# Kernel optimization log

Hardware: AMD Instinct MI355X
Metric: run time of the kernel (lower is better)

## Reference

```python
import jax, jax.numpy as jnp
import numpy as np

SCALE_REACH = 10.0   # 'scale' in forward
SCALE_COS = 16.0     # CosNorm_Classifier default scale


def setup_inputs() -> dict:
    key = jax.random.key(0)
    ks = jax.random.split(key, 7)
    B, C, F = 64, 1000, 2048
    return {
        "x": jax.random.normal(ks[0], (B, F), jnp.float32),
        "centroids": jax.random.normal(ks[1], (C, F), jnp.float32),
        "W_hall": jax.random.normal(ks[2], (C, F), jnp.float32) * 0.02,
        "b_hall": jax.random.normal(ks[3], (C,), jnp.float32) * 0.02,
        "W_sel": jax.random.normal(ks[4], (F, F), jnp.float32) * 0.02,
        "b_sel": jax.random.normal(ks[5], (F,), jnp.float32) * 0.02,
        "W_cos": jax.random.normal(ks[6], (C, F), jnp.float32) * 0.001,
    }


def reference(x, centroids, W_hall, b_hall, W_sel, b_sel, W_cos):
    direct_feature = x
    # L2 distance to every class centroid: [B, C] (materializes [B, C, F] diff as in torch)
    diff = x[:, None, :] - centroids[None, :, :]
    dist = jnp.sqrt(jnp.sum(diff * diff, axis=2))
    # original sorts then takes column 0 -> min distance
    min_dist = jnp.min(dist, axis=1)                      # [B]
    reachability = (SCALE_REACH / min_dist)[:, None]      # [B, 1], broadcast over feat

    # hallucinated memory read
    values_memory = jax.nn.softmax(x @ W_hall.T + b_hall, axis=1)  # [B, C]
    memory_feature = values_memory @ centroids                      # [B, F]

    concept_selector = jnp.tanh(x @ W_sel.T + b_sel)                # [B, F]
    infused_feature = concept_selector * memory_feature
    feat = reachability * (direct_feature + infused_feature)

    # CosNorm classifier
    norm_x = jnp.linalg.norm(feat, axis=1, keepdims=True)           # [B, 1]
    ex = (norm_x / (1.0 + norm_x)) * (feat / norm_x)                # norm-gated unit vec
    ew = W_cos / jnp.linalg.norm(W_cos, axis=1, keepdims=True)      # [C, F]
    logits = ex @ (ew.T * SCALE_COS)                                # [B, C]

    return logits, direct_feature, infused_feature
```

## Files before the change

kernel.cpp:

```cpp
#include <hip/hip_runtime.h>
#include <math.h>

#define FF 2048

typedef __attribute__((ext_vector_type(8))) short short8;
typedef __attribute__((ext_vector_type(4))) float floatx4;

#define OFF_SPART 0
#define OFF_HPART 1024000
#define OFF_SELP  2048000
#define OFF_MEMP  4145152
#define OFF_LOGP  5193728
#define OFF_V     7241728
#define OFF_FEAT  7307264
#define OFF_CN2   7438336
#define OFF_WINV  7439336
#define OFF_XN2   7440336
#define OFF_REACH 7440400
#define OFF_NRM2P 7440464

#define TP 40

__device__ __forceinline__ void split2(float f, ushort& h, ushort& l) {
  unsigned u = __float_as_uint(f);
  float r = f - __uint_as_float(u & 0xffff0000u);
  h = (ushort)(u >> 16);
  l = (ushort)(__float_as_uint(r) >> 16);
}

struct R2 { float4 a, b; };

__device__ __forceinline__ void load_bt(const float* __restrict__ M, int ldK, int rowBase,
                                        int nrows, int k0, R2& s, int t) {
  int r = t >> 2, q = t & 3;
  int grow = rowBase + r;
  const float* src = M + (size_t)grow * ldK + k0 + q * 8;
  s.a = make_float4(0.f, 0.f, 0.f, 0.f);
  s.b = s.a;
  if (grow < nrows) {
    s.a = *(const float4*)src;
    s.b = *(const float4*)(src + 4);
  }
}

__device__ __forceinline__ void store_bt(const R2& s, ushort* __restrict__ hi,
                                         ushort* __restrict__ lo, int t) {
  int r = t >> 2, q = t & 3;
#pragma unroll
  for (int h = 0; h < 2; ++h) {
    const float4& v = h ? s.b : s.a;
    ushort4 hv, lv;
    split2(v.x, hv.x, lv.x); split2(v.y, hv.y, lv.y);
    split2(v.z, hv.z, lv.z); split2(v.w, hv.w, lv.w);
    int base = r * TP + q * 8 + h * 4;
    *(ushort4*)(hi + base) = hv;
    *(ushort4*)(lo + base) = lv;
  }
}

__device__ __forceinline__ void load_tr(const float* __restrict__ M, int ldN, int k0, int kmax,
                                        int n0, R2& s, int t) {
  int kk = t >> 3, c8 = (t & 7) * 8;
  int gk = k0 + kk;
  const float* src = M + (size_t)gk * ldN + n0 + c8;
  s.a = make_float4(0.f, 0.f, 0.f, 0.f);
  s.b = s.a;
  if (gk < kmax) {
    s.a = *(const float4*)src;
    s.b = *(const float4*)(src + 4);
  }
}

__device__ __forceinline__ void store_tr(const R2& s, ushort* __restrict__ hi,
                                         ushort* __restrict__ lo, int t) {
  int kk = t >> 3, c8 = (t & 7) * 8;
#pragma unroll
  for (int j = 0; j < 8; ++j) {
    float f = (j < 4) ? ((const float*)&s.a)[j] : ((const float*)&s.b)[j - 4];
    ushort h, l;
    split2(f, h, l);
    hi[(c8 + j) * TP + kk] = h;
    lo[(c8 + j) * TP + kk] = l;
  }
}

#define MFMA(a, b, c) __builtin_amdgcn_mfma_f32_16x16x32_bf16(a, b, c, 0, 0, 0)

__device__ __forceinline__ void mfma_tile(const ushort* __restrict__ Ah, const ushort* __restrict__ Al,
                                          const ushort* __restrict__ Bh, const ushort* __restrict__ Bl,
                                          int ln15, int q8, int mh, int nh, floatx4 (&acc)[2][2]) {
  short8 ah[2], al[2];
#pragma unroll
  for (int i = 0; i < 2; ++i) {
    int row = (mh * 2 + i) * 16 + ln15;
    ah[i] = *(const short8*)(Ah + row * TP + q8);
    al[i] = *(const short8*)(Al + row * TP + q8);
  }
#pragma unroll
  for (int j = 0; j < 2; ++j) {
    int brow = (nh * 2 + j) * 16 + ln15;
    short8 bh = *(const short8*)(Bh + brow * TP + q8);
    short8 bl = *(const short8*)(Bl + brow * TP + q8);
#pragma unroll
    for (int i = 0; i < 2; ++i) {
      acc[i][j] = MFMA(ah[i], bh, acc[i][j]);
      acc[i][j] = MFMA(ah[i], bl, acc[i][j]);
      acc[i][j] = MFMA(al[i], bh, acc[i][j]);
    }
  }
}

__global__ __launch_bounds__(256) void k1_gemm1(
    const float* __restrict__ x, const float* __restrict__ cent,
    const float* __restrict__ whall, const float* __restrict__ wcos,
    float* __restrict__ ws) {
  __shared__ __align__(16) ushort u_lds[4 * 64 * TP];
  ushort* Ah = u_lds;
  ushort* Al = u_lds + 64 * TP;
  ushort* Bh = u_lds + 2 * 64 * TP;
  ushort* Bl = u_lds + 3 * 64 * TP;
  int bx = blockIdx.x, t = threadIdx.x;
  int lane = t & 63, w = t >> 6;
  int ln15 = t & 15, lq = (t >> 4) & 3, q8 = lq * 8;
  int mh = w & 1, nh = w >> 1;

  for (int r = bx * 4 + w; r < 2064; r += 2048) {
    const float* src = (r < 1000) ? cent + (size_t)r * FF
                     : (r < 2000) ? wcos + (size_t)(r - 1000) * FF
                                  : x + (size_t)(r - 2000) * FF;
    float s = 0.f;
#pragma unroll
    for (int i = 0; i < 8; ++i) {
      float4 v = *(const float4*)(src + i * 256 + lane * 4);
      s += v.x * v.x + v.y * v.y + v.z * v.z + v.w * v.w;
    }
#pragma unroll
    for (int off = 32; off > 0; off >>= 1) s += __shfl_down(s, off, 64);
    if (lane == 0) {
      if (r < 1000) ws[OFF_CN2 + r] = s;
      else if (r < 2000) ws[OFF_WINV + (r - 1000)] = 1.f / sqrtf(s);
      else ws[OFF_XN2 + (r - 2000)] = s;
    }
  }

  int mat = bx >> 8;
  int ks = (bx >> 4) & 15;
  int tile = bx & 15;
  int n0 = tile * 64;
  const float* Bm = mat ? whall : cent;
  float* outp = ws + (mat ? OFF_HPART : OFF_SPART) + (size_t)ks * 64000;

  floatx4 acc[2][2];
#pragma unroll
  for (int i = 0; i < 2; ++i)
#pragma unroll
    for (int j = 0; j < 2; ++j) acc[i][j] = (floatx4){0.f, 0.f, 0.f, 0.f};

  R2 rA[2], rB[2];
  load_bt(x,  FF, 0,  64,   ks * 128,      rA[0], t);
  load_bt(Bm, FF, n0, 1000, ks * 128,      rB[0], t);
  load_bt(x,  FF, 0,  64,   ks * 128 + 32, rA[1], t);
  load_bt(Bm, FF, n0, 1000, ks * 128 + 32, rB[1], t);
#pragma unroll
  for (int kc = 0; kc < 4; ++kc) {
    __syncthreads();
    store_bt(rA[kc & 1], Ah, Al, t);
    store_bt(rB[kc & 1], Bh, Bl, t);
    if (kc + 2 < 4) {
      load_bt(x,  FF, 0,  64,   ks * 128 + (kc + 2) * 32, rA[kc & 1], t);
      load_bt(Bm, FF, n0, 1000, ks * 128 + (kc + 2) * 32, rB[kc & 1], t);
    }
    __syncthreads();
    mfma_tile(Ah, Al, Bh, Bl, ln15, q8, mh, nh, acc);
  }
#pragma unroll
  for (int i = 0; i < 2; ++i)
#pragma unroll
    for (int j = 0; j < 2; ++j) {
      int gn = n0 + (nh * 2 + j) * 16 + ln15;
      if (gn < 1000) {
#pragma unroll
        for (int r = 0; r < 4; ++r) {
          int gm = (mh * 2 + i) * 16 + lq * 4 + r;
          outp[gm * 1000 + gn] = acc[i][j][r];
        }
      }
    }
}

__global__ __launch_bounds__(256) void k2_softmax(const float* __restrict__ bhall,
                                                  float* __restrict__ ws) {
  __shared__ float hrow[1000];
  __shared__ float red[256];
  int b = blockIdx.x, t = threadIdx.x;
  float xn = ws[OFF_XN2 + b];
  float lmin = 3.0e38f, lmax = -3.0e38f;
  if (t < 250) {
    int c0 = t * 4;
    floatx4 S = {0.f, 0.f, 0.f, 0.f}, H = {0.f, 0.f, 0.f, 0.f};
#pragma unroll
    for (int ks = 0; ks < 16; ++ks) {
      floatx4 sv = *(const floatx4*)(ws + OFF_SPART + (size_t)ks * 64000 + b * 1000 + c0);
      floatx4 hv = *(const floatx4*)(ws + OFF_HPART + (size_t)ks * 64000 + b * 1000 + c0);
      S += sv; H += hv;
    }
    floatx4 bh = *(const floatx4*)(bhall + c0);
    floatx4 cn = *(const floatx4*)(ws + OFF_CN2 + c0);
#pragma unroll
    for (int j = 0; j < 4; ++j) {
      float Hf = H[j] + bh[j];
      hrow[c0 + j] = Hf;
      float d2 = xn - 2.f * S[j] + cn[j];
      lmin = fminf(lmin, d2);
      lmax = fmaxf(lmax, Hf);
    }
  }
  red[t] = lmin; __syncthreads();
  for (int s = 128; s > 0; s >>= 1) { if (t < s) red[t] = fminf(red[t], red[t + s]); __syncthreads(); }
  float bmin = red[0]; __syncthreads();
  red[t] = lmax; __syncthreads();
  for (int s = 128; s > 0; s >>= 1) { if (t < s) red[t] = fmaxf(red[t], red[t + s]); __syncthreads(); }
  float bmax = red[0]; __syncthreads();
  float lsum = 0.f;
  float e4[4] = {0.f, 0.f, 0.f, 0.f};
  if (t < 250) {
#pragma unroll
    for (int j = 0; j < 4; ++j) {
      e4[j] = expf(hrow[t * 4 + j] - bmax);
      lsum += e4[j];
    }
  }
  red[t] = lsum; __syncthreads();
  for (int s = 128; s > 0; s >>= 1) { if (t < s) red[t] += red[t + s]; __syncthreads(); }
  float inv = 1.f / red[0];
  if (t < 250)
    *(floatx4*)(ws + OFF_V + b * 1024 + t * 4) =
        (floatx4){e4[0] * inv, e4[1] * inv, e4[2] * inv, e4[3] * inv};
  if (t == 250) {
#pragma unroll
    for (int j = 0; j < 24; ++j) ws[OFF_V + b * 1024 + 1000 + j] = 0.f;
  }
  if (t == 0) ws[OFF_REACH + b] = 10.f / sqrtf(bmin);
}

__global__ __launch_bounds__(256) void k3_memsel(const float* __restrict__ x,
                                                 const float* __restrict__ cent,
                                                 const float* __restrict__ wsel,
                                                 float* __restrict__ ws) {
  __shared__ __align__(16) ushort u_lds[4 * 64 * TP];
  ushort* Ah = u_lds;
  ushort* Al = u_lds + 64 * TP;
  ushort* Bh = u_lds + 2 * 64 * TP;
  ushort* Bl = u_lds + 3 * 64 * TP;
  int bx = blockIdx.x, t = threadIdx.x;
  int ln15 = t & 15, lq = (t >> 4) & 3, q8 = lq * 8;
  int w = t >> 6, mh = w & 1, nh = w >> 1;

  floatx4 acc[2][2];
#pragma unroll
  for (int i = 0; i < 2; ++i)
#pragma unroll
    for (int j = 0; j < 2; ++j) acc[i][j] = (floatx4){0.f, 0.f, 0.f, 0.f};

  if (bx < 256) {
    int tile = bx & 31, ks = bx >> 5;
    int n0 = tile * 64;
    const float* V = ws + OFF_V;
    R2 rA[2], rB[2];
    load_bt(V, 1024, 0, 64, ks * 128,      rA[0], t);
    load_tr(cent, FF, ks * 128,      1000, n0, rB[0], t);
    load_bt(V, 1024, 0, 64, ks * 128 + 32, rA[1], t);
    load_tr(cent, FF, ks * 128 + 32, 1000, n0, rB[1], t);
#pragma unroll
    for (int kc = 0; kc < 4; ++kc) {
      __syncthreads();
      store_bt(rA[kc & 1], Ah, Al, t);
      store_tr(rB[kc & 1], Bh, Bl, t);
      if (kc + 2 < 4) {
        load_bt(V, 1024, 0, 64, ks * 128 + (kc + 2) * 32, rA[kc & 1], t);
        load_tr(cent, FF, ks * 128 + (kc + 2) * 32, 1000, n0, rB[kc & 1], t);
      }
      __syncthreads();
      mfma_tile(Ah, Al, Bh, Bl, ln15, q8, mh, nh, acc);
    }
    float* memp = ws + OFF_MEMP + (size_t)ks * 131072;
#pragma unroll
    for (int i = 0; i < 2; ++i)
#pragma unroll
      for (int j = 0; j < 2; ++j) {
        int gn = n0 + (nh * 2 + j) * 16 + ln15;
#pragma unroll
        for (int r = 0; r < 4; ++r) {
          int gm = (mh * 2 + i) * 16 + lq * 4 + r;
          memp[gm * 2048 + gn] = acc[i][j][r];
        }
      }
  } else {
    int b2 = bx - 256;
    int tile = b2 & 31, ks = b2 >> 5;
    int n0 = tile * 64;
    R2 rA[2], rB[2];
    load_bt(x,    FF, 0,  64,   ks * 128,      rA[0], t);
    load_bt(wsel, FF, n0, 2048, ks * 128,      rB[0], t);
    load_bt(x,    FF, 0,  64,   ks * 128 + 32, rA[1], t);
    load_bt(wsel, FF, n0, 2048, ks * 128 + 32, rB[1], t);
#pragma unroll
    for (int kc = 0; kc < 4; ++kc) {
      __syncthreads();
      store_bt(rA[kc & 1], Ah, Al, t);
      store_bt(rB[kc & 1], Bh, Bl, t);
      if (kc + 2 < 4) {
        load_bt(x,    FF, 0,  64,   ks * 128 + (kc + 2) * 32, rA[kc & 1], t);
        load_bt(wsel, FF, n0, 2048, ks * 128 + (kc + 2) * 32, rB[kc & 1], t);
      }
      __syncthreads();
      mfma_tile(Ah, Al, Bh, Bl, ln15, q8, mh, nh, acc);
    }
    float* selp = ws + OFF_SELP + (size_t)ks * 131072;
#pragma unroll
    for (int i = 0; i < 2; ++i)
#pragma unroll
      for (int j = 0; j < 2; ++j) {
        int gn = n0 + (nh * 2 + j) * 16 + ln15;
#pragma unroll
        for (int r = 0; r < 4; ++r) {
          int gm = (mh * 2 + i) * 16 + lq * 4 + r;
          selp[gm * 2048 + gn] = acc[i][j][r];
        }
      }
  }
}

__global__ __launch_bounds__(64) void k4_fuse(const float* __restrict__ x,
                                              const float* __restrict__ bsel,
                                              float* __restrict__ ws, float* __restrict__ out) {
  int bx = blockIdx.x, t = threadIdx.x;
  int row = bx >> 3, ch = bx & 7;
  int f = ch * 256 + t * 4;
  const float* selp = ws + OFF_SELP + (size_t)row * 2048 + f;
  const float* memp = ws + OFF_MEMP + (size_t)row * 2048 + f;
  floatx4 sp = {0.f, 0.f, 0.f, 0.f}, mm = {0.f, 0.f, 0.f, 0.f};
#pragma unroll
  for (int ks = 0; ks < 16; ++ks)
    sp += *(const floatx4*)(selp + (size_t)ks * 131072);
#pragma unroll
  for (int ks = 0; ks < 8; ++ks)
    mm += *(const floatx4*)(memp + (size_t)ks * 131072);
  float4 bs4 = *(const float4*)(bsel + f);
  float4 x4  = *(const float4*)(x + (size_t)row * 2048 + f);
  float rch = ws[OFF_REACH + row];
  float4 inf4;
  floatx4 ft4;
  float nrm2 = 0.f;
#pragma unroll
  for (int j = 0; j < 4; ++j) {
    float sel = tanhf(sp[j] + ((float*)&bs4)[j]);
    float inf = sel * mm[j];
    float ft = rch * (((float*)&x4)[j] + inf);
    ((float*)&inf4)[j] = inf;
    ft4[j] = ft;
    nrm2 += ft * ft;
  }
  *(float4*)(out + 64000 + (size_t)row * 2048 + f) = x4;
  *(float4*)(out + 195072 + (size_t)row * 2048 + f) = inf4;
  *(floatx4*)(ws + OFF_FEAT + (size_t)row * 2048 + f) = ft4;
#pragma unroll
  for (int off = 32; off > 0; off >>= 1) nrm2 += __shfl_down(nrm2, off, 64);
  if (t == 0) ws[OFF_NRM2P + row * 8 + ch] = nrm2;
}

__global__ __launch_bounds__(256) void k5_logits(const float* __restrict__ wcos,
                                                 float* __restrict__ ws) {
  __shared__ __align__(16) ushort u_lds[4 * 64 * TP];
  ushort* Ah = u_lds;
  ushort* Al = u_lds + 64 * TP;
  ushort* Bh = u_lds + 2 * 64 * TP;
  ushort* Bl = u_lds + 3 * 64 * TP;
  int bx = blockIdx.x, t = threadIdx.x;
  int tile = bx & 15, ks = bx >> 4;
  int n0 = tile * 64;
  int ln15 = t & 15, lq = (t >> 4) & 3, q8 = lq * 8;
  int w = t >> 6, mh = w & 1, nh = w >> 1;
  const float* feat = ws + OFF_FEAT;

  floatx4 acc[2][2];
#pragma unroll
  for (int i = 0; i < 2; ++i)
#pragma unroll
    for (int j = 0; j < 2; ++j) acc[i][j] = (floatx4){0.f, 0.f, 0.f, 0.f};

  R2 rA[2], rB[2];
  load_bt(feat, FF, 0,  64,   ks * 64,      rA[0], t);
  load_bt(wcos, FF, n0, 1000, ks * 64,      rB[0], t);
  load_bt(feat, FF, 0,  64,   ks * 64 + 32, rA[1], t);
  load_bt(wcos, FF, n0, 1000, ks * 64 + 32, rB[1], t);
#pragma unroll
  for (int kc = 0; kc < 2; ++kc) {
    __syncthreads();
    store_bt(rA[kc], Ah, Al, t);
    store_bt(rB[kc], Bh, Bl, t);
    __syncthreads();
    mfma_tile(Ah, Al, Bh, Bl, ln15, q8, mh, nh, acc);
  }
  float* logp = ws + OFF_LOGP + (size_t)ks * 64000;
#pragma unroll
  for (int i = 0; i < 2; ++i)
#pragma unroll
    for (int j = 0; j < 2; ++j) {
      int gn = n0 + (nh * 2 + j) * 16 + ln15;
      if (gn < 1000) {
#pragma unroll
        for (int r = 0; r < 4; ++r) {
          int gm = (mh * 2 + i) * 16 + lq * 4 + r;
          logp[gm * 1000 + gn] = acc[i][j][r];
        }
      }
    }
}

__global__ __launch_bounds__(128) void k6_final(float* __restrict__ ws, float* __restrict__ out) {
  int bx = blockIdx.x, t = threadIdx.x;
  int idx0 = (bx * 128 + t) * 4;
  const float* logp = ws + OFF_LOGP + idx0;
  floatx4 s = {0.f, 0.f, 0.f, 0.f};
#pragma unroll
  for (int ks = 0; ks < 32; ++ks)
    s += *(const floatx4*)(logp + (size_t)ks * 64000);
  floatx4 o4;
  int pb = -1;
  float sfac = 0.f;
#pragma unroll
  for (int j = 0; j < 4; ++j) {
    int idx = idx0 + j;
    int bb = idx / 1000;
    int cc = idx - bb * 1000;
    if (bb != pb) {
      float n2 = 0.f;
#pragma unroll
      for (int q = 0; q < 8; ++q) n2 += ws[OFF_NRM2P + bb * 8 + q];
      sfac = 16.f / (1.f + sqrtf(n2));
      pb = bb;
    }
    o4[j] = s[j] * sfac * ws[OFF_WINV + cc];
  }
  *(floatx4*)(out + idx0) = o4;
}

extern "C" void kernel_launch(void* const* d_in, const int* in_sizes, int n_in,
                              void* d_out, int out_size, void* d_ws, size_t ws_size,
                              hipStream_t stream) {
  const float* x     = (const float*)d_in[0];
  const float* cent  = (const float*)d_in[1];
  const float* whall = (const float*)d_in[2];
  const float* bhall = (const float*)d_in[3];
  const float* wsel  = (const float*)d_in[4];
  const float* bsel  = (const float*)d_in[5];
  const float* wcos  = (const float*)d_in[6];
  float* out = (float*)d_out;
  float* ws  = (float*)d_ws;

  hipLaunchKernelGGL(k1_gemm1,   dim3(512), dim3(256), 0, stream, x, cent, whall, wcos, ws);
  hipLaunchKernelGGL(k2_softmax, dim3(64),  dim3(256), 0, stream, bhall, ws);
  hipLaunchKernelGGL(k3_memsel,  dim3(768), dim3(256), 0, stream, x, cent, wsel, ws);
  hipLaunchKernelGGL(k4_fuse,    dim3(512), dim3(64),  0, stream, x, bsel, ws, out);
  hipLaunchKernelGGL(k5_logits,  dim3(512), dim3(256), 0, stream, wcos, ws);
  hipLaunchKernelGGL(k6_final,   dim3(125), dim3(128), 0, stream, ws, out);
}
```

Measured before the change: 122.0 us.

## Load GEMM operands directly to registers and move selector GEMM into first kernel

Adds a register-direct GEMM path that loads fp32 operands from global memory straight into MFMA fragment layout and splits them to bf16 hi/lo in registers. This removes the LDS staging and block barriers in the x·W_hall, x·centroids, x·W_sel and logits GEMMs. The x·W_sel GEMM moves from the third kernel into the first, where it does not depend on the softmax. Split-K counts are halved, so partial-sum buffers shrink and the reduction loops shorten, but each block now does more serial K work and gets no operand reuse across waves through LDS.

```diff
diff --git a/kernel.cpp b/kernel.cpp
--- a/kernel.cpp
+++ b/kernel.cpp
@@ -7,17 +7,17 @@
 typedef __attribute__((ext_vector_type(4))) float floatx4;
 
 #define OFF_SPART 0
-#define OFF_HPART 1024000
-#define OFF_SELP  2048000
-#define OFF_MEMP  4145152
-#define OFF_LOGP  5193728
-#define OFF_V     7241728
-#define OFF_FEAT  7307264
-#define OFF_CN2   7438336
-#define OFF_WINV  7439336
-#define OFF_XN2   7440336
-#define OFF_REACH 7440400
-#define OFF_NRM2P 7440464
+#define OFF_HPART 512000
+#define OFF_SELP  1024000
+#define OFF_MEMP  2072576
+#define OFF_LOGP  3121152
+#define OFF_V     4145152
+#define OFF_FEAT  4210688
+#define OFF_CN2   4341760
+#define OFF_WINV  4342760
+#define OFF_XN2   4343760
+#define OFF_REACH 4343824
+#define OFF_NRM2P 4343888
 
 #define TP 40
 
@@ -26,6 +26,91 @@
   float r = f - __uint_as_float(u & 0xffff0000u);
   h = (ushort)(u >> 16);
   l = (ushort)(__float_as_uint(r) >> 16);
+}
+
+__device__ __forceinline__ void cvt8(const float4& a, const float4& b, short8& hi, short8& lo) {
+  const float* f0 = (const float*)&a;
+  const float* f1 = (const float*)&b;
+  short8 h, l;
+#pragma unroll
+  for (int j = 0; j < 4; ++j) {
+    ushort hh, ll;
+    split2(f0[j], hh, ll);
+    h[j] = (short)hh; l[j] = (short)ll;
+    split2(f1[j], hh, ll);
+    h[j + 4] = (short)hh; l[j + 4] = (short)ll;
+  }
+  hi = h; lo = l;
+}
+
+#define MFMA(a, b, c) __builtin_amdgcn_mfma_f32_16x16x32_bf16(a, b, c, 0, 0, 0)
+
+__device__ __forceinline__ void mfma_step(const short8 (&ah)[2], const short8 (&al)[2],
+                                          const short8 (&bh)[2], const short8 (&bl)[2],
+                                          floatx4 (&acc)[2][2]) {
+#pragma unroll
+  for (int j = 0; j < 2; ++j)
+#pragma unroll
+    for (int i = 0; i < 2; ++i) {
+      acc[i][j] = MFMA(ah[i], bh[j], acc[i][j]);
+      acc[i][j] = MFMA(ah[i], bl[j], acc[i][j]);
+      acc[i][j] = MFMA(al[i], bh[j], acc[i][j]);
+    }
+}
+
+template<int NSTEPS>
+__device__ __forceinline__ void gemm_direct(
+    const float* __restrict__ A, int ldA,
+    const float* __restrict__ B, int ldB,
+    int n0, int nB, int kbase,
+    int ln15, int kq, int mh, int nh,
+    floatx4 (&acc)[2][2]) {
+  const float* pa[2];
+  const float* pb[2];
+  bool okb[2];
+#pragma unroll
+  for (int i = 0; i < 2; ++i) {
+    int ra = (mh * 2 + i) * 16 + ln15;
+    pa[i] = A + (size_t)ra * ldA + kbase + kq;
+    int rb = n0 + (nh * 2 + i) * 16 + ln15;
+    okb[i] = rb < nB;
+    pb[i] = B + (size_t)rb * ldB + kbase + kq;
+  }
+  float4 ca[2][2], cb[2][2], na[2][2], nb[2][2];
+#pragma unroll
+  for (int i = 0; i < 2; ++i) {
+    ca[i][0] = *(const float4*)(pa[i]);
+    ca[i][1] = *(const float4*)(pa[i] + 4);
+    cb[i][0] = make_float4(0.f, 0.f, 0.f, 0.f); cb[i][1] = cb[i][0];
+    if (okb[i]) { cb[i][0] = *(const float4*)(pb[i]); cb[i][1] = *(const float4*)(pb[i] + 4); }
+  }
+#pragma unroll
+  for (int s = 0; s < NSTEPS; ++s) {
+    if (s + 1 < NSTEPS) {
+      int off = (s + 1) * 32;
+#pragma unroll
+      for (int i = 0; i < 2; ++i) {
+        na[i][0] = *(const float4*)(pa[i] + off);
+        na[i][1] = *(const float4*)(pa[i] + off + 4);
+        nb[i][0] = make_float4(0.f, 0.f, 0.f, 0.f); nb[i][1] = nb[i][0];
+        if (okb[i]) { nb[i][0] = *(const float4*)(pb[i] + off); nb[i][1] = *(const float4*)(pb[i] + off + 4); }
+      }
+    }
+    short8 ah[2], al[2], bh[2], bl[2];
+#pragma unroll
+    for (int i = 0; i < 2; ++i) {
+      cvt8(ca[i][0], ca[i][1], ah[i], al[i]);
+      cvt8(cb[i][0], cb[i][1], bh[i], bl[i]);
+    }
+    mfma_step(ah, al, bh, bl, acc);
+    if (s + 1 < NSTEPS) {
+#pragma unroll
+      for (int i = 0; i < 2; ++i) {
+        ca[i][0] = na[i][0]; ca[i][1] = na[i][1];
+        cb[i][0] = nb[i][0]; cb[i][1] = nb[i][1];
+      }
+    }
+  }
 }
 
 struct R2 { float4 a, b; };
@@ -84,8 +169,6 @@
   }
 }
 
-#define MFMA(a, b, c) __builtin_amdgcn_mfma_f32_16x16x32_bf16(a, b, c, 0, 0, 0)
-
 __device__ __forceinline__ void mfma_tile(const ushort* __restrict__ Ah, const ushort* __restrict__ Al,
                                           const ushort* __restrict__ Bh, const ushort* __restrict__ Bl,
                                           int ln15, int q8, int mh, int nh, floatx4 (&acc)[2][2]) {
@@ -112,16 +195,11 @@
 
 __global__ __launch_bounds__(256) void k1_gemm1(
     const float* __restrict__ x, const float* __restrict__ cent,
-    const float* __restrict__ whall, const float* __restrict__ wcos,
-    float* __restrict__ ws) {
-  __shared__ __align__(16) ushort u_lds[4 * 64 * TP];
-  ushort* Ah = u_lds;
-  ushort* Al = u_lds + 64 * TP;
-  ushort* Bh = u_lds + 2 * 64 * TP;
-  ushort* Bl = u_lds + 3 * 64 * TP;
+    const float* __restrict__ whall, const float* __restrict__ wsel,
+    const float* __restrict__ wcos, float* __restrict__ ws) {
   int bx = blockIdx.x, t = threadIdx.x;
   int lane = t & 63, w = t >> 6;
-  int ln15 = t & 15, lq = (t >> 4) & 3, q8 = lq * 8;
+  int ln15 = t & 15, lq = (t >> 4) & 3, kq = lq * 8;
   int mh = w & 1, nh = w >> 1;
 
   for (int r = bx * 4 + w; r < 2064; r += 2048) {
@@ -143,49 +221,51 @@
     }
   }
 
-  int mat = bx >> 8;
-  int ks = (bx >> 4) & 15;
-  int tile = bx & 15;
-  int n0 = tile * 64;
-  const float* Bm = mat ? whall : cent;
-  float* outp = ws + (mat ? OFF_HPART : OFF_SPART) + (size_t)ks * 64000;
-
   floatx4 acc[2][2];
 #pragma unroll
   for (int i = 0; i < 2; ++i)
 #pragma unroll
     for (int j = 0; j < 2; ++j) acc[i][j] = (floatx4){0.f, 0.f, 0.f, 0.f};
 
-  R2 rA[2], rB[2];
-  load_bt(x,  FF, 0,  64,   ks * 128,      rA[0], t);
-  load_bt(Bm, FF, n0, 1000, ks * 128,      rB[0], t);
-  load_bt(x,  FF, 0,  64,   ks * 128 + 32, rA[1], t);
-  load_bt(Bm, FF, n0, 1000, ks * 128 + 32, rB[1], t);
-#pragma unroll
-  for (int kc = 0; kc < 4; ++kc) {
-    __syncthreads();
-    store_bt(rA[kc & 1], Ah, Al, t);
-    store_bt(rB[kc & 1], Bh, Bl, t);
-    if (kc + 2 < 4) {
-      load_bt(x,  FF, 0,  64,   ks * 128 + (kc + 2) * 32, rA[kc & 1], t);
-      load_bt(Bm, FF, n0, 1000, ks * 128 + (kc + 2) * 32, rB[kc & 1], t);
-    }
-    __syncthreads();
-    mfma_tile(Ah, Al, Bh, Bl, ln15, q8, mh, nh, acc);
-  }
-#pragma unroll
-  for (int i = 0; i < 2; ++i)
-#pragma unroll
-    for (int j = 0; j < 2; ++j) {
-      int gn = n0 + (nh * 2 + j) * 16 + ln15;
-      if (gn < 1000) {
+  if (bx < 256) {
+    int mat = bx >> 7;
+    int b2 = bx & 127;
+    int tile = b2 & 15, ks = b2 >> 4;
+    int n0 = tile * 64;
+    const float* Bm = mat ? whall : cent;
+    gemm_direct<8>(x, FF, Bm, FF, n0, 1000, ks * 256, ln15, kq, mh, nh, acc);
+    float* outp = ws + (mat ? OFF_HPART : OFF_SPART) + (size_t)ks * 64000;
+#pragma unroll
+    for (int i = 0; i < 2; ++i)
+#pragma unroll
+      for (int j = 0; j < 2; ++j) {
+        int gn = n0 + (nh * 2 + j) * 16 + ln15;
+        if (gn < 1000) {
+#pragma unroll
+          for (int r = 0; r < 4; ++r) {
+            int gm = (mh * 2 + i) * 16 + lq * 4 + r;
+            outp[gm * 1000 + gn] = acc[i][j][r];
+          }
+        }
+      }
+  } else {
+    int b2 = bx - 256;
+    int tile = b2 & 31, ks = b2 >> 5;
+    int n0 = tile * 64;
+    gemm_direct<8>(x, FF, wsel, FF, n0, 2048, ks * 256, ln15, kq, mh, nh, acc);
+    float* selp = ws + OFF_SELP + (size_t)ks * 131072;
+#pragma unroll
+    for (int i = 0; i < 2; ++i)
+#pragma unroll
+      for (int j = 0; j < 2; ++j) {
+        int gn = n0 + (nh * 2 + j) * 16 + ln15;
 #pragma unroll
         for (int r = 0; r < 4; ++r) {
           int gm = (mh * 2 + i) * 16 + lq * 4 + r;
-          outp[gm * 1000 + gn] = acc[i][j][r];
+          selp[gm * 2048 + gn] = acc[i][j][r];
         }
       }
-    }
+  }
 }
 
 __global__ __launch_bounds__(256) void k2_softmax(const float* __restrict__ bhall,
@@ -199,7 +279,7 @@
     int c0 = t * 4;
     floatx4 S = {0.f, 0.f, 0.f, 0.f}, H = {0.f, 0.f, 0.f, 0.f};
 #pragma unroll
-    for (int ks = 0; ks < 16; ++ks) {
+    for (int ks = 0; ks < 8; ++ks) {
       floatx4 sv = *(const floatx4*)(ws + OFF_SPART + (size_t)ks * 64000 + b * 1000 + c0);
       floatx4 hv = *(const floatx4*)(ws + OFF_HPART + (size_t)ks * 64000 + b * 1000 + c0);
       S += sv; H += hv;
@@ -243,10 +323,8 @@
   if (t == 0) ws[OFF_REACH + b] = 10.f / sqrtf(bmin);
 }
 
-__global__ __launch_bounds__(256) void k3_memsel(const float* __restrict__ x,
-                                                 const float* __restrict__ cent,
-                                                 const float* __restrict__ wsel,
-                                                 float* __restrict__ ws) {
+__global__ __launch_bounds__(256) void k3_mem(const float* __restrict__ cent,
+                                              float* __restrict__ ws) {
   __shared__ __align__(16) ushort u_lds[4 * 64 * TP];
   ushort* Ah = u_lds;
   ushort* Al = u_lds + 64 * TP;
@@ -255,6 +333,9 @@
   int bx = blockIdx.x, t = threadIdx.x;
   int ln15 = t & 15, lq = (t >> 4) & 3, q8 = lq * 8;
   int w = t >> 6, mh = w & 1, nh = w >> 1;
+  int tile = bx & 31, ks = bx >> 5;
+  int n0 = tile * 64;
+  const float* V = ws + OFF_V;
 
   floatx4 acc[2][2];
 #pragma unroll
@@ -262,73 +343,35 @@
 #pragma unroll
     for (int j = 0; j < 2; ++j) acc[i][j] = (floatx4){0.f, 0.f, 0.f, 0.f};
 
-  if (bx < 256) {
-    int tile = bx & 31, ks = bx >> 5;
-    int n0 = tile * 64;
-    const float* V = ws + OFF_V;
-    R2 rA[2], rB[2];
-    load_bt(V, 1024, 0, 64, ks * 128,      rA[0], t);
-    load_tr(cent, FF, ks * 128,      1000, n0, rB[0], t);
-    load_bt(V, 1024, 0, 64, ks * 128 + 32, rA[1], t);
-    load_tr(cent, FF, ks * 128 + 32, 1000, n0, rB[1], t);
-#pragma unroll
-    for (int kc = 0; kc < 4; ++kc) {
-      __syncthreads();
-      store_bt(rA[kc & 1], Ah, Al, t);
-      store_tr(rB[kc & 1], Bh, Bl, t);
-      if (kc + 2 < 4) {
-        load_bt(V, 1024, 0, 64, ks * 128 + (kc + 2) * 32, rA[kc & 1], t);
-        load_tr(cent, FF, ks * 128 + (kc + 2) * 32, 1000, n0, rB[kc & 1], t);
-      }
-      __syncthreads();
-      mfma_tile(Ah, Al, Bh, Bl, ln15, q8, mh, nh, acc);
-    }
-    float* memp = ws + OFF_MEMP + (size_t)ks * 131072;
-#pragma unroll
-    for (int i = 0; i < 2; ++i)
-#pragma unroll
-      for (int j = 0; j < 2; ++j) {
-        int gn = n0 + (nh * 2 + j) * 16 + ln15;
-#pragma unroll
-        for (int r = 0; r < 4; ++r) {
-          int gm = (mh * 2 + i) * 16 + lq * 4 + r;
-          memp[gm * 2048 + gn] = acc[i][j][r];
-        }
-      }
-  } else {
-    int b2 = bx - 256;
-    int tile = b2 & 31, ks = b2 >> 5;
-    int n0 = tile * 64;
-    R2 rA[2], rB[2];
-    load_bt(x,    FF, 0,  64,   ks * 128,      rA[0], t);
-    load_bt(wsel, FF, n0, 2048, ks * 128,      rB[0], t);
-    load_bt(x,    FF, 0,  64,   ks * 128 + 32, rA[1], t);
-    load_bt(wsel, FF, n0, 2048, ks * 128 + 32, rB[1], t);
-#pragma unroll
-    for (int kc = 0; kc < 4; ++kc) {
-      __syncthreads();
-      store_bt(rA[kc & 1], Ah, Al, t);
-      store_bt(rB[kc & 1], Bh, Bl, t);
-      if (kc + 2 < 4) {
-        load_bt(x,    FF, 0,  64,   ks * 128 + (kc + 2) * 32, rA[kc & 1], t);
-        load_bt(wsel, FF, n0, 2048, ks * 128 + (kc + 2) * 32, rB[kc & 1], t);
-      }
-      __syncthreads();
-      mfma_tile(Ah, Al, Bh, Bl, ln15, q8, mh, nh, acc);
-    }
-    float* selp = ws + OFF_SELP + (size_t)ks * 131072;
-#pragma unroll
-    for (int i = 0; i < 2; ++i)
-#pragma unroll
-      for (int j = 0; j < 2; ++j) {
-        int gn = n0 + (nh * 2 + j) * 16 + ln15;
-#pragma unroll
-        for (int r = 0; r < 4; ++r) {
-          int gm = (mh * 2 + i) * 16 + lq * 4 + r;
-          selp[gm * 2048 + gn] = acc[i][j][r];
-        }
-      }
-  }
+  R2 rA[2], rB[2];
+  load_bt(V, 1024, 0, 64, ks * 128,      rA[0], t);
+  load_tr(cent, FF, ks * 128,      1000, n0, rB[0], t);
+  load_bt(V, 1024, 0, 64, ks * 128 + 32, rA[1], t);
+  load_tr(cent, FF, ks * 128 + 32, 1000, n0, rB[1], t);
+#pragma unroll
+  for (int kc = 0; kc < 4; ++kc) {
+    __syncthreads();
+    store_bt(rA[kc & 1], Ah, Al, t);
+    store_tr(rB[kc & 1], Bh, Bl, t);
+    if (kc + 2 < 4) {
+      load_bt(V, 1024, 0, 64, ks * 128 + (kc + 2) * 32, rA[kc & 1], t);
+      load_tr(cent, FF, ks * 128 + (kc + 2) * 32, 1000, n0, rB[kc & 1], t);
+    }
+    __syncthreads();
+    mfma_tile(Ah, Al, Bh, Bl, ln15, q8, mh, nh, acc);
+  }
+  float* memp = ws + OFF_MEMP + (size_t)ks * 131072;
+#pragma unroll
+  for (int i = 0; i < 2; ++i)
+#pragma unroll
+    for (int j = 0; j < 2; ++j) {
+      int gn = n0 + (nh * 2 + j) * 16 + ln15;
+#pragma unroll
+      for (int r = 0; r < 4; ++r) {
+        int gm = (mh * 2 + i) * 16 + lq * 4 + r;
+        memp[gm * 2048 + gn] = acc[i][j][r];
+      }
+    }
 }
 
 __global__ __launch_bounds__(64) void k4_fuse(const float* __restrict__ x,
@@ -341,11 +384,10 @@
   const float* memp = ws + OFF_MEMP + (size_t)row * 2048 + f;
   floatx4 sp = {0.f, 0.f, 0.f, 0.f}, mm = {0.f, 0.f, 0.f, 0.f};
 #pragma unroll
-  for (int ks = 0; ks < 16; ++ks)
+  for (int ks = 0; ks < 8; ++ks) {
     sp += *(const floatx4*)(selp + (size_t)ks * 131072);
-#pragma unroll
-  for (int ks = 0; ks < 8; ++ks)
     mm += *(const floatx4*)(memp + (size_t)ks * 131072);
+  }
   float4 bs4 = *(const float4*)(bsel + f);
   float4 x4  = *(const float4*)(x + (size_t)row * 2048 + f);
   float rch = ws[OFF_REACH + row];
@@ -371,15 +413,10 @@
 
 __global__ __launch_bounds__(256) void k5_logits(const float* __restrict__ wcos,
                                                  float* __restrict__ ws) {
-  __shared__ __align__(16) ushort u_lds[4 * 64 * TP];
-  ushort* Ah = u_lds;
-  ushort* Al = u_lds + 64 * TP;
-  ushort* Bh = u_lds + 2 * 64 * TP;
-  ushort* Bl = u_lds + 3 * 64 * TP;
   int bx = blockIdx.x, t = threadIdx.x;
   int tile = bx & 15, ks = bx >> 4;
   int n0 = tile * 64;
-  int ln15 = t & 15, lq = (t >> 4) & 3, q8 = lq * 8;
+  int ln15 = t & 15, lq = (t >> 4) & 3, kq = lq * 8;
   int w = t >> 6, mh = w & 1, nh = w >> 1;
   const float* feat = ws + OFF_FEAT;
 
@@ -389,19 +426,8 @@
 #pragma unroll
     for (int j = 0; j < 2; ++j) acc[i][j] = (floatx4){0.f, 0.f, 0.f, 0.f};
 
-  R2 rA[2], rB[2];
-  load_bt(feat, FF, 0,  64,   ks * 64,      rA[0], t);
-  load_bt(wcos, FF, n0, 1000, ks * 64,      rB[0], t);
-  load_bt(feat, FF, 0,  64,   ks * 64 + 32, rA[1], t);
-  load_bt(wcos, FF, n0, 1000, ks * 64 + 32, rB[1], t);
-#pragma unroll
-  for (int kc = 0; kc < 2; ++kc) {
-    __syncthreads();
-    store_bt(rA[kc], Ah, Al, t);
-    store_bt(rB[kc], Bh, Bl, t);
-    __syncthreads();
-    mfma_tile(Ah, Al, Bh, Bl, ln15, q8, mh, nh, acc);
-  }
+  gemm_direct<4>(feat, FF, wcos, FF, n0, 1000, ks * 128, ln15, kq, mh, nh, acc);
+
   float* logp = ws + OFF_LOGP + (size_t)ks * 64000;
 #pragma unroll
   for (int i = 0; i < 2; ++i)
@@ -424,7 +450,7 @@
   const float* logp = ws + OFF_LOGP + idx0;
   floatx4 s = {0.f, 0.f, 0.f, 0.f};
 #pragma unroll
-  for (int ks = 0; ks < 32; ++ks)
+  for (int ks = 0; ks < 16; ++ks)
     s += *(const floatx4*)(logp + (size_t)ks * 64000);
   floatx4 o4;
   int pb = -1;
@@ -459,10 +485,10 @@
   float* out = (float*)d_out;
   float* ws  = (float*)d_ws;
 
-  hipLaunchKernelGGL(k1_gemm1,   dim3(512), dim3(256), 0, stream, x, cent, whall, wcos, ws);
+  hipLaunchKernelGGL(k1_gemm1,   dim3(512), dim3(256), 0, stream, x, cent, whall, wsel, wcos, ws);
   hipLaunchKernelGGL(k2_softmax, dim3(64),  dim3(256), 0, stream, bhall, ws);
-  hipLaunchKernelGGL(k3_memsel,  dim3(768), dim3(256), 0, stream, x, cent, wsel, ws);
+  hipLaunchKernelGGL(k3_mem,     dim3(256), dim3(256), 0, stream, cent, ws);
   hipLaunchKernelGGL(k4_fuse,    dim3(512), dim3(64),  0, stream, x, bsel, ws, out);
-  hipLaunchKernelGGL(k5_logits,  dim3(512), dim3(256), 0, stream, wcos, ws);
+  hipLaunchKernelGGL(k5_logits,  dim3(256), dim3(256), 0, stream, wcos, ws);
   hipLaunchKernelGGL(k6_final,   dim3(125), dim3(128), 0, stream, ws, out);
 }
```

Result: slower. 128.7 us (+5.5%).

## Move x@W_sel GEMM into first kernel and double split-K for distance/hall GEMMs

Applied to the files above, without the earlier changes.

The independent x@W_sel^T GEMM moves from the post-softmax kernel into the first kernel, so it runs alongside the distance and hallucination GEMMs instead of after the softmax. Split-K is doubled (32 slices of 64 for the first GEMMs, 16 for the memory GEMM) to create more blocks. The softmax now uses 1024 threads with scalar loads, and the final reduction is made scalar. This adds more partial-sum traffic and larger workspace, and the softmax and final kernels give up vectorized loads.

```diff
diff --git a/kernel.cpp b/kernel.cpp
--- a/kernel.cpp
+++ b/kernel.cpp
@@ -7,17 +7,17 @@
 typedef __attribute__((ext_vector_type(4))) float floatx4;
 
 #define OFF_SPART 0
-#define OFF_HPART 1024000
-#define OFF_SELP  2048000
-#define OFF_MEMP  4145152
-#define OFF_LOGP  5193728
-#define OFF_V     7241728
-#define OFF_FEAT  7307264
-#define OFF_CN2   7438336
-#define OFF_WINV  7439336
-#define OFF_XN2   7440336
-#define OFF_REACH 7440400
-#define OFF_NRM2P 7440464
+#define OFF_HPART 2048000
+#define OFF_SELP  4096000
+#define OFF_MEMP  6193152
+#define OFF_LOGP  8290304
+#define OFF_V     10338304
+#define OFF_FEAT  10403840
+#define OFF_CN2   10534912
+#define OFF_WINV  10535912
+#define OFF_XN2   10536912
+#define OFF_REACH 10536976
+#define OFF_NRM2P 10537040
 
 #define TP 40
 
@@ -112,8 +112,8 @@
 
 __global__ __launch_bounds__(256) void k1_gemm1(
     const float* __restrict__ x, const float* __restrict__ cent,
-    const float* __restrict__ whall, const float* __restrict__ wcos,
-    float* __restrict__ ws) {
+    const float* __restrict__ whall, const float* __restrict__ wsel,
+    const float* __restrict__ wcos, float* __restrict__ ws) {
   __shared__ __align__(16) ushort u_lds[4 * 64 * TP];
   ushort* Ah = u_lds;
   ushort* Al = u_lds + 64 * TP;
@@ -124,7 +124,8 @@
   int ln15 = t & 15, lq = (t >> 4) & 3, q8 = lq * 8;
   int mh = w & 1, nh = w >> 1;
 
-  for (int r = bx * 4 + w; r < 2064; r += 2048) {
+  int r = bx * 4 + w;
+  if (r < 2064) {
     const float* src = (r < 1000) ? cent + (size_t)r * FF
                      : (r < 2000) ? wcos + (size_t)(r - 1000) * FF
                                   : x + (size_t)(r - 2000) * FF;
@@ -143,160 +144,47 @@
     }
   }
 
-  int mat = bx >> 8;
-  int ks = (bx >> 4) & 15;
-  int tile = bx & 15;
-  int n0 = tile * 64;
-  const float* Bm = mat ? whall : cent;
-  float* outp = ws + (mat ? OFF_HPART : OFF_SPART) + (size_t)ks * 64000;
-
   floatx4 acc[2][2];
 #pragma unroll
   for (int i = 0; i < 2; ++i)
 #pragma unroll
     for (int j = 0; j < 2; ++j) acc[i][j] = (floatx4){0.f, 0.f, 0.f, 0.f};
 
-  R2 rA[2], rB[2];
-  load_bt(x,  FF, 0,  64,   ks * 128,      rA[0], t);
-  load_bt(Bm, FF, n0, 1000, ks * 128,      rB[0], t);
-  load_bt(x,  FF, 0,  64,   ks * 128 + 32, rA[1], t);
-  load_bt(Bm, FF, n0, 1000, ks * 128 + 32, rB[1], t);
-#pragma unroll
-  for (int kc = 0; kc < 4; ++kc) {
-    __syncthreads();
-    store_bt(rA[kc & 1], Ah, Al, t);
-    store_bt(rB[kc & 1], Bh, Bl, t);
-    if (kc + 2 < 4) {
-      load_bt(x,  FF, 0,  64,   ks * 128 + (kc + 2) * 32, rA[kc & 1], t);
-      load_bt(Bm, FF, n0, 1000, ks * 128 + (kc + 2) * 32, rB[kc & 1], t);
-    }
-    __syncthreads();
-    mfma_tile(Ah, Al, Bh, Bl, ln15, q8, mh, nh, acc);
-  }
-#pragma unroll
-  for (int i = 0; i < 2; ++i)
-#pragma unroll
-    for (int j = 0; j < 2; ++j) {
-      int gn = n0 + (nh * 2 + j) * 16 + ln15;
-      if (gn < 1000) {
-#pragma unroll
-        for (int r = 0; r < 4; ++r) {
-          int gm = (mh * 2 + i) * 16 + lq * 4 + r;
-          outp[gm * 1000 + gn] = acc[i][j][r];
-        }
-      }
-    }
-}
-
-__global__ __launch_bounds__(256) void k2_softmax(const float* __restrict__ bhall,
-                                                  float* __restrict__ ws) {
-  __shared__ float hrow[1000];
-  __shared__ float red[256];
-  int b = blockIdx.x, t = threadIdx.x;
-  float xn = ws[OFF_XN2 + b];
-  float lmin = 3.0e38f, lmax = -3.0e38f;
-  if (t < 250) {
-    int c0 = t * 4;
-    floatx4 S = {0.f, 0.f, 0.f, 0.f}, H = {0.f, 0.f, 0.f, 0.f};
-#pragma unroll
-    for (int ks = 0; ks < 16; ++ks) {
-      floatx4 sv = *(const floatx4*)(ws + OFF_SPART + (size_t)ks * 64000 + b * 1000 + c0);
-      floatx4 hv = *(const floatx4*)(ws + OFF_HPART + (size_t)ks * 64000 + b * 1000 + c0);
-      S += sv; H += hv;
-    }
-    floatx4 bh = *(const floatx4*)(bhall + c0);
-    floatx4 cn = *(const floatx4*)(ws + OFF_CN2 + c0);
-#pragma unroll
-    for (int j = 0; j < 4; ++j) {
-      float Hf = H[j] + bh[j];
-      hrow[c0 + j] = Hf;
-      float d2 = xn - 2.f * S[j] + cn[j];
-      lmin = fminf(lmin, d2);
-      lmax = fmaxf(lmax, Hf);
-    }
-  }
-  red[t] = lmin; __syncthreads();
-  for (int s = 128; s > 0; s >>= 1) { if (t < s) red[t] = fminf(red[t], red[t + s]); __syncthreads(); }
-  float bmin = red[0]; __syncthreads();
-  red[t] = lmax; __syncthreads();
-  for (int s = 128; s > 0; s >>= 1) { if (t < s) red[t] = fmaxf(red[t], red[t + s]); __syncthreads(); }
-  float bmax = red[0]; __syncthreads();
-  float lsum = 0.f;
-  float e4[4] = {0.f, 0.f, 0.f, 0.f};
-  if (t < 250) {
-#pragma unroll
-    for (int j = 0; j < 4; ++j) {
-      e4[j] = expf(hrow[t * 4 + j] - bmax);
-      lsum += e4[j];
-    }
-  }
-  red[t] = lsum; __syncthreads();
-  for (int s = 128; s > 0; s >>= 1) { if (t < s) red[t] += red[t + s]; __syncthreads(); }
-  float inv = 1.f / red[0];
-  if (t < 250)
-    *(floatx4*)(ws + OFF_V + b * 1024 + t * 4) =
-        (floatx4){e4[0] * inv, e4[1] * inv, e4[2] * inv, e4[3] * inv};
-  if (t == 250) {
-#pragma unroll
-    for (int j = 0; j < 24; ++j) ws[OFF_V + b * 1024 + 1000 + j] = 0.f;
-  }
-  if (t == 0) ws[OFF_REACH + b] = 10.f / sqrtf(bmin);
-}
-
-__global__ __launch_bounds__(256) void k3_memsel(const float* __restrict__ x,
-                                                 const float* __restrict__ cent,
-                                                 const float* __restrict__ wsel,
-                                                 float* __restrict__ ws) {
-  __shared__ __align__(16) ushort u_lds[4 * 64 * TP];
-  ushort* Ah = u_lds;
-  ushort* Al = u_lds + 64 * TP;
-  ushort* Bh = u_lds + 2 * 64 * TP;
-  ushort* Bl = u_lds + 3 * 64 * TP;
-  int bx = blockIdx.x, t = threadIdx.x;
-  int ln15 = t & 15, lq = (t >> 4) & 3, q8 = lq * 8;
-  int w = t >> 6, mh = w & 1, nh = w >> 1;
-
-  floatx4 acc[2][2];
-#pragma unroll
-  for (int i = 0; i < 2; ++i)
-#pragma unroll
-    for (int j = 0; j < 2; ++j) acc[i][j] = (floatx4){0.f, 0.f, 0.f, 0.f};
-
-  if (bx < 256) {
-    int tile = bx & 31, ks = bx >> 5;
+  if (bx < 1024) {
+    int mat = bx >> 9;
+    int b2 = bx & 511;
+    int tile = b2 & 15, ks = b2 >> 4;
     int n0 = tile * 64;
-    const float* V = ws + OFF_V;
+    const float* Bm = mat ? whall : cent;
     R2 rA[2], rB[2];
-    load_bt(V, 1024, 0, 64, ks * 128,      rA[0], t);
-    load_tr(cent, FF, ks * 128,      1000, n0, rB[0], t);
-    load_bt(V, 1024, 0, 64, ks * 128 + 32, rA[1], t);
-    load_tr(cent, FF, ks * 128 + 32, 1000, n0, rB[1], t);
-#pragma unroll
-    for (int kc = 0; kc < 4; ++kc) {
+    load_bt(x,  FF, 0,  64,   ks * 64,      rA[0], t);
+    load_bt(Bm, FF, n0, 1000, ks * 64,      rB[0], t);
+    load_bt(x,  FF, 0,  64,   ks * 64 + 32, rA[1], t);
+    load_bt(Bm, FF, n0, 1000, ks * 64 + 32, rB[1], t);
+#pragma unroll
+    for (int kc = 0; kc < 2; ++kc) {
       __syncthreads();
-      store_bt(rA[kc & 1], Ah, Al, t);
-      store_tr(rB[kc & 1], Bh, Bl, t);
-      if (kc + 2 < 4) {
-        load_bt(V, 1024, 0, 64, ks * 128 + (kc + 2) * 32, rA[kc & 1], t);
-        load_tr(cent, FF, ks * 128 + (kc + 2) * 32, 1000, n0, rB[kc & 1], t);
-      }
+      store_bt(rA[kc], Ah, Al, t);
+      store_bt(rB[kc], Bh, Bl, t);
       __syncthreads();
       mfma_tile(Ah, Al, Bh, Bl, ln15, q8, mh, nh, acc);
     }
-    float* memp = ws + OFF_MEMP + (size_t)ks * 131072;
+    float* outp = ws + (mat ? OFF_HPART : OFF_SPART) + (size_t)ks * 64000;
 #pragma unroll
     for (int i = 0; i < 2; ++i)
 #pragma unroll
       for (int j = 0; j < 2; ++j) {
         int gn = n0 + (nh * 2 + j) * 16 + ln15;
-#pragma unroll
-        for (int r = 0; r < 4; ++r) {
-          int gm = (mh * 2 + i) * 16 + lq * 4 + r;
-          memp[gm * 2048 + gn] = acc[i][j][r];
+        if (gn < 1000) {
+#pragma unroll
+          for (int rr = 0; rr < 4; ++rr) {
+            int gm = (mh * 2 + i) * 16 + lq * 4 + rr;
+            outp[gm * 1000 + gn] = acc[i][j][rr];
+          }
         }
       }
   } else {
-    int b2 = bx - 256;
+    int b2 = bx - 1024;
     int tile = b2 & 31, ks = b2 >> 5;
     int n0 = tile * 64;
     R2 rA[2], rB[2];
@@ -323,12 +211,92 @@
       for (int j = 0; j < 2; ++j) {
         int gn = n0 + (nh * 2 + j) * 16 + ln15;
 #pragma unroll
-        for (int r = 0; r < 4; ++r) {
-          int gm = (mh * 2 + i) * 16 + lq * 4 + r;
-          selp[gm * 2048 + gn] = acc[i][j][r];
+        for (int rr = 0; rr < 4; ++rr) {
+          int gm = (mh * 2 + i) * 16 + lq * 4 + rr;
+          selp[gm * 2048 + gn] = acc[i][j][rr];
         }
       }
   }
+}
+
+__global__ __launch_bounds__(1024) void k2_softmax(const float* __restrict__ bhall,
+                                                   float* __restrict__ ws) {
+  __shared__ float red[1024];
+  int b = blockIdx.x, t = threadIdx.x;
+  float xn = ws[OFF_XN2 + b];
+  float lmin = 3.0e38f, lmax = -3.0e38f;
+  float Hf = 0.f;
+  if (t < 1000) {
+    float S = 0.f, H = 0.f;
+#pragma unroll
+    for (int ks = 0; ks < 32; ++ks) {
+      S += ws[OFF_SPART + (size_t)ks * 64000 + b * 1000 + t];
+      H += ws[OFF_HPART + (size_t)ks * 64000 + b * 1000 + t];
+    }
+    Hf = H + bhall[t];
+    float d2 = xn - 2.f * S + ws[OFF_CN2 + t];
+    lmin = d2;
+    lmax = Hf;
+  }
+  red[t] = lmin; __syncthreads();
+  for (int s = 512; s > 0; s >>= 1) { if (t < s) red[t] = fminf(red[t], red[t + s]); __syncthreads(); }
+  float bmin = red[0]; __syncthreads();
+  red[t] = lmax; __syncthreads();
+  for (int s = 512; s > 0; s >>= 1) { if (t < s) red[t] = fmaxf(red[t], red[t + s]); __syncthreads(); }
+  float bmax = red[0]; __syncthreads();
+  float e = (t < 1000) ? expf(Hf - bmax) : 0.f;
+  red[t] = e; __syncthreads();
+  for (int s = 512; s > 0; s >>= 1) { if (t < s) red[t] += red[t + s]; __syncthreads(); }
+  float inv = 1.f / red[0];
+  ws[OFF_V + b * 1024 + t] = e * inv;
+  if (t == 0) ws[OFF_REACH + b] = 10.f / sqrtf(bmin);
+}
+
+__global__ __launch_bounds__(256) void k3_mem(const float* __restrict__ cent,
+                                              float* __restrict__ ws) {
+  __shared__ __align__(16) ushort u_lds[4 * 64 * TP];
+  ushort* Ah = u_lds;
+  ushort* Al = u_lds + 64 * TP;
+  ushort* Bh = u_lds + 2 * 64 * TP;
+  ushort* Bl = u_lds + 3 * 64 * TP;
+  int bx = blockIdx.x, t = threadIdx.x;
+  int ln15 = t & 15, lq = (t >> 4) & 3, q8 = lq * 8;
+  int w = t >> 6, mh = w & 1, nh = w >> 1;
+  int tile = bx & 31, ks = bx >> 5;
+  int n0 = tile * 64;
+  const float* V = ws + OFF_V;
+
+  floatx4 acc[2][2];
+#pragma unroll
+  for (int i = 0; i < 2; ++i)
+#pragma unroll
+    for (int j = 0; j < 2; ++j) acc[i][j] = (floatx4){0.f, 0.f, 0.f, 0.f};
+
+  R2 rA[2], rB[2];
+  load_bt(V, 1024, 0, 64, ks * 64,      rA[0], t);
+  load_tr(cent, FF, ks * 64,      1000, n0, rB[0], t);
+  load_bt(V, 1024, 0, 64, ks * 64 + 32, rA[1], t);
+  load_tr(cent, FF, ks * 64 + 32, 1000, n0, rB[1], t);
+#pragma unroll
+  for (int kc = 0; kc < 2; ++kc) {
+    __syncthreads();
+    store_bt(rA[kc], Ah, Al, t);
+    store_tr(rB[kc], Bh, Bl, t);
+    __syncthreads();
+    mfma_tile(Ah, Al, Bh, Bl, ln15, q8, mh, nh, acc);
+  }
+  float* memp = ws + OFF_MEMP + (size_t)ks * 131072;
+#pragma unroll
+  for (int i = 0; i < 2; ++i)
+#pragma unroll
+    for (int j = 0; j < 2; ++j) {
+      int gn = n0 + (nh * 2 + j) * 16 + ln15;
+#pragma unroll
+      for (int rr = 0; rr < 4; ++rr) {
+        int gm = (mh * 2 + i) * 16 + lq * 4 + rr;
+        memp[gm * 2048 + gn] = acc[i][j][rr];
+      }
+    }
 }
 
 __global__ __launch_bounds__(64) void k4_fuse(const float* __restrict__ x,
@@ -341,11 +309,10 @@
   const float* memp = ws + OFF_MEMP + (size_t)row * 2048 + f;
   floatx4 sp = {0.f, 0.f, 0.f, 0.f}, mm = {0.f, 0.f, 0.f, 0.f};
 #pragma unroll
-  for (int ks = 0; ks < 16; ++ks)
+  for (int ks = 0; ks < 16; ++ks) {
     sp += *(const floatx4*)(selp + (size_t)ks * 131072);
-#pragma unroll
-  for (int ks = 0; ks < 8; ++ks)
     mm += *(const floatx4*)(memp + (size_t)ks * 131072);
+  }
   float4 bs4 = *(const float4*)(bsel + f);
   float4 x4  = *(const float4*)(x + (size_t)row * 2048 + f);
   float rch = ws[OFF_REACH + row];
@@ -410,40 +377,28 @@
       int gn = n0 + (nh * 2 + j) * 16 + ln15;
       if (gn < 1000) {
 #pragma unroll
-        for (int r = 0; r < 4; ++r) {
-          int gm = (mh * 2 + i) * 16 + lq * 4 + r;
-          logp[gm * 1000 + gn] = acc[i][j][r];
+        for (int rr = 0; rr < 4; ++rr) {
+          int gm = (mh * 2 + i) * 16 + lq * 4 + rr;
+          logp[gm * 1000 + gn] = acc[i][j][rr];
         }
       }
     }
 }
 
 __global__ __launch_bounds__(128) void k6_final(float* __restrict__ ws, float* __restrict__ out) {
-  int bx = blockIdx.x, t = threadIdx.x;
-  int idx0 = (bx * 128 + t) * 4;
-  const float* logp = ws + OFF_LOGP + idx0;
-  floatx4 s = {0.f, 0.f, 0.f, 0.f};
+  int idx = blockIdx.x * 128 + threadIdx.x;
+  const float* logp = ws + OFF_LOGP + idx;
+  float s = 0.f;
 #pragma unroll
   for (int ks = 0; ks < 32; ++ks)
-    s += *(const floatx4*)(logp + (size_t)ks * 64000);
-  floatx4 o4;
-  int pb = -1;
-  float sfac = 0.f;
-#pragma unroll
-  for (int j = 0; j < 4; ++j) {
-    int idx = idx0 + j;
-    int bb = idx / 1000;
-    int cc = idx - bb * 1000;
-    if (bb != pb) {
-      float n2 = 0.f;
-#pragma unroll
-      for (int q = 0; q < 8; ++q) n2 += ws[OFF_NRM2P + bb * 8 + q];
-      sfac = 16.f / (1.f + sqrtf(n2));
-      pb = bb;
-    }
-    o4[j] = s[j] * sfac * ws[OFF_WINV + cc];
-  }
-  *(floatx4*)(out + idx0) = o4;
+    s += logp[(size_t)ks * 64000];
+  int bb = idx / 1000;
+  int cc = idx - bb * 1000;
+  float n2 = 0.f;
+#pragma unroll
+  for (int q = 0; q < 8; ++q) n2 += ws[OFF_NRM2P + bb * 8 + q];
+  float sfac = 16.f / (1.f + sqrtf(n2));
+  out[idx] = s * sfac * ws[OFF_WINV + cc];
 }
 
 extern "C" void kernel_launch(void* const* d_in, const int* in_sizes, int n_in,
@@ -459,10 +414,10 @@
   float* out = (float*)d_out;
   float* ws  = (float*)d_ws;
 
-  hipLaunchKernelGGL(k1_gemm1,   dim3(512), dim3(256), 0, stream, x, cent, whall, wcos, ws);
-  hipLaunchKernelGGL(k2_softmax, dim3(64),  dim3(256), 0, stream, bhall, ws);
-  hipLaunchKernelGGL(k3_memsel,  dim3(768), dim3(256), 0, stream, x, cent, wsel, ws);
-  hipLaunchKernelGGL(k4_fuse,    dim3(512), dim3(64),  0, stream, x, bsel, ws, out);
-  hipLaunchKernelGGL(k5_logits,  dim3(512), dim3(256), 0, stream, wcos, ws);
-  hipLaunchKernelGGL(k6_final,   dim3(125), dim3(128), 0, stream, ws, out);
-}
+  hipLaunchKernelGGL(k1_gemm1,   dim3(1536), dim3(256),  0, stream, x, cent, whall, wsel, wcos, ws);
+  hipLaunchKernelGGL(k2_softmax, dim3(64),   dim3(1024), 0, stream, bhall, ws);
+  hipLaunchKernelGGL(k3_mem,     dim3(512),  dim3(256),  0, stream, cent, ws);
+  hipLaunchKernelGGL(k4_fuse,    dim3(512),  dim3(64),   0, stream, x, bsel, ws, out);
+  hipLaunchKernelGGL(k5_logits,  dim3(512),  dim3(256),  0, stream, wcos, ws);
+  hipLaunchKernelGGL(k6_final,   dim3(500),  dim3(128),  0, stream, ws, out);
+}
```

After: 142.6 us. +16.8%, slower.
